# Optimization experiments

Hardware: AMD Instinct MI355X
Metric: run time of the kernel (lower is better)

Reference implementation:

```python
import jax, jax.numpy as jnp
import numpy as np

NUM_HEADS = 10
LN_EPS = 1e-5

def setup_inputs() -> dict:
    key = jax.random.key(0)
    ks = jax.random.split(key, 8)
    B, H, N, D, Dt = 256, 200, 64, 640, 256
    s = 0.02
    return {
        'clicked_news': jax.random.normal(ks[0], (B, H, D), jnp.float32),
        'clicked_topics': jax.random.normal(ks[1], (B, H, Dt), jnp.float32),
        'cand_topics': jax.random.normal(ks[2], (B, N, Dt), jnp.float32),
        'Wq': jax.random.normal(ks[3], (D, Dt), jnp.float32) * s,
        'bq': jnp.zeros((D,), jnp.float32),
        'Wk': jax.random.normal(ks[4], (D, Dt), jnp.float32) * s,
        'bk': jnp.zeros((D,), jnp.float32),
        'Wv': jax.random.normal(ks[5], (D, D), jnp.float32) * s,
        'bv': jnp.zeros((D,), jnp.float32),
        'Wg': jax.random.normal(ks[6], (D, D), jnp.float32) * s,
        'bg': jnp.zeros((D,), jnp.float32),
        'ln_gamma': jnp.ones((D,), jnp.float32),
        'ln_beta': jnp.zeros((D,), jnp.float32),
    }

def reference(clicked_news, clicked_topics, cand_topics, Wq, bq, Wk, bk, Wv, bv, Wg, bg, ln_gamma, ln_beta):
    B, H, D = clicked_news.shape
    N = cand_topics.shape[1]
    nh = NUM_HEADS
    hd = D // nh
    scale = jnp.sqrt(jnp.asarray(D, clicked_news.dtype))

    Qf = cand_topics @ Wq.T + bq            # [B, N, D]
    Kf = clicked_topics @ Wk.T + bk         # [B, H, D]
    # V projection feeds `weighted`, which is dead code w.r.t. outputs; omitted.

    Q = Qf.reshape(B, N, nh, hd)
    K = Kf.reshape(B, H, nh, hd)
    scores = jnp.einsum('bnhd,bmhd->bhnm', Q, K) / scale   # [B, nh, N, H]
    attn = jax.nn.softmax(scores, axis=-1)                 # dropout is identity in eval

    # query weighting: softmax over candidates of ||Q||
    query_weights = jax.nn.softmax(jnp.linalg.norm(Qf, axis=-1), axis=1)   # [B, N]
    agg = (attn.sum(axis=1) * query_weights[:, :, None]).sum(axis=1)       # [B, H]
    attn_weights_agg = jax.nn.softmax(agg, axis=-1)                        # [B, H]

    weighted_clicked = attn_weights_agg[:, :, None] * clicked_news         # [B, H, D]
    gate = jax.nn.sigmoid(weighted_clicked @ Wg.T + bg)
    out = gate * weighted_clicked + (1.0 - gate) * clicked_news

    mu = out.mean(axis=-1, keepdims=True)
    var = out.var(axis=-1, keepdims=True)
    out = (out - mu) / jnp.sqrt(var + LN_EPS) * ln_gamma + ln_beta
    return out, attn_weights_agg
```

## Files before the change

kernel.cpp:

```cpp
#include <hip/hip_runtime.h>
#include <math.h>

#define B_  256
#define H_  200
#define N_  64
#define D_  640
#define DT_ 256
#define NH_ 10
#define HD_ 64
#define MT_ 13

typedef __attribute__((ext_vector_type(8))) short bf16x8;
typedef __attribute__((ext_vector_type(4))) float f32x4;

__device__ __forceinline__ float wave_reduce_sum(float v) {
    #pragma unroll
    for (int m = 32; m > 0; m >>= 1) v += __shfl_xor(v, m);
    return v;
}
__device__ __forceinline__ float wave_reduce_max(float v) {
    #pragma unroll
    for (int m = 32; m > 0; m >>= 1) v = fmaxf(v, __shfl_xor(v, m));
    return v;
}
__device__ __forceinline__ float red16_sum(float v) {
    #pragma unroll
    for (int m = 1; m < 16; m <<= 1) v += __shfl_xor(v, m);
    return v;
}
__device__ __forceinline__ float red16_max(float v) {
    #pragma unroll
    for (int m = 1; m < 16; m <<= 1) v = fmaxf(v, __shfl_xor(v, m));
    return v;
}
__device__ __forceinline__ short f2bf(float x) {
    unsigned u = __float_as_uint(x);
    unsigned r = (u + 0x7fffu + ((u >> 16) & 1u)) >> 16;
    return (short)r;
}
__device__ __forceinline__ float bf2f(short s) {
    return __uint_as_float(((unsigned)(unsigned short)s) << 16);
}
#define SWZ(row, byte) ((byte) ^ (((row) & 7) << 4))

__global__ __launch_bounds__(256) void convert_w(
    const float* __restrict__ src, short* __restrict__ dst, int n)
{
    for (int i = blockIdx.x * 256 + threadIdx.x; i < n; i += gridDim.x * 256)
        dst[i] = f2bf(src[i]);
}

__global__ __launch_bounds__(512, 2) void proj_mfma(
    const float* __restrict__ X, const short* __restrict__ Wb,
    const float* __restrict__ bias, short* __restrict__ Y)
{
    __shared__ short A_lds[64 * DT_];
    const int t = threadIdx.x;
    const int lane = t & 63, w = t >> 6;
    const int r16 = lane & 15, g = lane >> 4;
    const long row0 = (long)blockIdx.x * 64;

    const float4* X4 = (const float4*)(X + row0 * DT_);
    for (int i = t; i < 64 * (DT_ / 4); i += 512) {
        float4 v = X4[i];
        int row = i / (DT_ / 4);
        int k4  = i % (DT_ / 4);
        short4 s;
        s.x = f2bf(v.x); s.y = f2bf(v.y); s.z = f2bf(v.z); s.w = f2bf(v.w);
        *(short4*)((char*)A_lds + SWZ(row, row * (DT_ * 2) + k4 * 8)) = s;
    }
    __syncthreads();

    f32x4 acc[5][4];
    #pragma unroll
    for (int ct = 0; ct < 5; ++ct)
        #pragma unroll
        for (int rt = 0; rt < 4; ++rt) acc[ct][rt] = (f32x4){0.f,0.f,0.f,0.f};

    const short* Wbase = Wb + (long)(w * 80 + r16) * DT_ + g * 8;
    #pragma unroll 2
    for (int kc = 0; kc < DT_ / 32; ++kc) {
        bf16x8 a[4];
        #pragma unroll
        for (int rt = 0; rt < 4; ++rt) {
            const int row = rt * 16 + r16;
            a[rt] = *(const bf16x8*)((const char*)A_lds +
                     SWZ(row, row * (DT_ * 2) + kc * 64 + g * 16));
        }
        bf16x8 bb[5];
        #pragma unroll
        for (int ct = 0; ct < 5; ++ct)
            bb[ct] = *(const bf16x8*)(Wbase + ct * 16 * DT_ + kc * 32);
        #pragma unroll
        for (int ct = 0; ct < 5; ++ct)
            #pragma unroll
            for (int rt = 0; rt < 4; ++rt)
                acc[ct][rt] = __builtin_amdgcn_mfma_f32_16x16x32_bf16(
                                  a[rt], bb[ct], acc[ct][rt], 0, 0, 0);
    }
    #pragma unroll
    for (int ct = 0; ct < 5; ++ct) {
        const int col = w * 80 + ct * 16 + r16;
        const float bv = bias[col];
        #pragma unroll
        for (int rt = 0; rt < 4; ++rt)
            #pragma unroll
            for (int i = 0; i < 4; ++i)
                Y[(row0 + rt * 16 + g * 4 + i) * (long)D_ + col] =
                    f2bf(acc[ct][rt][i] + bv);
    }
}

__global__ __launch_bounds__(256) void attn2(
    const short* __restrict__ Qb, const short* __restrict__ Kb,
    float* __restrict__ aw, float* __restrict__ out_tail)
{
    __shared__ float qn_l[N_];
    __shared__ float qw_l[N_];
    __shared__ float aggp[4][MT_ * 16];
    __shared__ float red2[2];
    const int t = threadIdx.x;
    const int lane = t & 63, wm = t >> 6;
    const int r16 = lane & 15, g = lane >> 4;
    const int b = blockIdx.x;

    {
        const short* qrow = Qb + ((long)(b * N_ + wm * 16 + r16)) * D_ + g * 160;
        float ss = 0.f;
        #pragma unroll
        for (int j = 0; j < 20; ++j) {
            bf16x8 v = *(const bf16x8*)(qrow + j * 8);
            #pragma unroll
            for (int e = 0; e < 8; ++e) { float f = bf2f(v[e]); ss += f * f; }
        }
        ss += __shfl_xor(ss, 16);
        ss += __shfl_xor(ss, 32);
        if (g == 0) qn_l[wm * 16 + r16] = ss;
    }
    __syncthreads();
    if (wm == 0) {
        float v = sqrtf(qn_l[lane]);
        float mx = wave_reduce_max(v);
        float e = __expf(v - mx);
        float s = wave_reduce_sum(e);
        qw_l[lane] = e / s;
    }
    __syncthreads();

    float qwr[4];
    #pragma unroll
    for (int i = 0; i < 4; ++i) qwr[i] = qw_l[wm * 16 + g * 4 + i];

    const float inv_scale = 0.0395284707521047f;
    float aggl[MT_];
    #pragma unroll
    for (int mt = 0; mt < MT_; ++mt) aggl[mt] = 0.f;

    for (int h = 0; h < NH_; ++h) {
        const short* qbase = Qb + ((long)(b * N_ + wm * 16 + r16)) * D_ + h * HD_ + g * 8;
        bf16x8 a0 = *(const bf16x8*)(qbase);
        bf16x8 a1 = *(const bf16x8*)(qbase + 32);
        f32x4 acc[MT_];
        #pragma unroll
        for (int mt = 0; mt < MT_; ++mt) {
            f32x4 z = {0.f,0.f,0.f,0.f};
            const short* kbase = Kb + ((long)(b * H_ + mt * 16 + r16)) * D_ + h * HD_ + g * 8;
            bf16x8 b0 = *(const bf16x8*)(kbase);
            bf16x8 b1 = *(const bf16x8*)(kbase + 32);
            z = __builtin_amdgcn_mfma_f32_16x16x32_bf16(a0, b0, z, 0, 0, 0);
            z = __builtin_amdgcn_mfma_f32_16x16x32_bf16(a1, b1, z, 0, 0, 0);
            acc[mt] = z;
        }
        const bool tailok = (r16 < 8);
        float mx[4] = {-INFINITY, -INFINITY, -INFINITY, -INFINITY};
        #pragma unroll
        for (int mt = 0; mt < MT_; ++mt) {
            const bool valid = (mt < 12) || tailok;
            #pragma unroll
            for (int i = 0; i < 4; ++i)
                if (valid) mx[i] = fmaxf(mx[i], acc[mt][i]);
        }
        #pragma unroll
        for (int i = 0; i < 4; ++i) mx[i] = red16_max(mx[i]);
        float sum[4] = {0.f, 0.f, 0.f, 0.f};
        #pragma unroll
        for (int mt = 0; mt < MT_; ++mt) {
            const bool valid = (mt < 12) || tailok;
            #pragma unroll
            for (int i = 0; i < 4; ++i) {
                float e = valid ? __expf((acc[mt][i] - mx[i]) * inv_scale) : 0.f;
                acc[mt][i] = e;
                sum[i] += e;
            }
        }
        float fct[4];
        #pragma unroll
        for (int i = 0; i < 4; ++i) fct[i] = qwr[i] / red16_sum(sum[i]);
        #pragma unroll
        for (int mt = 0; mt < MT_; ++mt)
            aggl[mt] += acc[mt][0] * fct[0] + acc[mt][1] * fct[1]
                      + acc[mt][2] * fct[2] + acc[mt][3] * fct[3];
    }
    #pragma unroll
    for (int mt = 0; mt < MT_; ++mt) {
        aggl[mt] += __shfl_xor(aggl[mt], 16);
        aggl[mt] += __shfl_xor(aggl[mt], 32);
    }
    if (g == 0) {
        #pragma unroll
        for (int mt = 0; mt < MT_; ++mt) aggp[wm][mt * 16 + r16] = aggl[mt];
    }
    __syncthreads();
    if (t < MT_ * 16) {
        float v = aggp[0][t] + aggp[1][t] + aggp[2][t] + aggp[3][t];
        aggp[0][t] = v;
    }
    __syncthreads();
    if (wm == 0) {
        float v0 = aggp[0][lane], v1 = aggp[0][lane + 64], v2 = aggp[0][lane + 128];
        const bool has3 = lane < (H_ - 192);
        float v3 = has3 ? aggp[0][lane + 192] : -INFINITY;
        float mx = wave_reduce_max(fmaxf(fmaxf(v0, v1), fmaxf(v2, v3)));
        float s = __expf(v0 - mx) + __expf(v1 - mx) + __expf(v2 - mx)
                + (has3 ? __expf(v3 - mx) : 0.f);
        s = wave_reduce_sum(s);
        if (lane == 0) { red2[0] = mx; red2[1] = s; }
    }
    __syncthreads();
    if (t < H_) {
        float v = __expf(aggp[0][t] - red2[0]) / red2[1];
        aw[b * H_ + t] = v;
        out_tail[b * H_ + t] = v;
    }
}

__global__ __launch_bounds__(512, 2) void out_mfma(
    const float* __restrict__ clicked, const float* __restrict__ aw,
    const short* __restrict__ Wgb, const float* __restrict__ bg,
    const float* __restrict__ gamma, const float* __restrict__ beta,
    float* __restrict__ out)
{
    __shared__ short A_lds[64 * D_];
    const int t = threadIdx.x;
    const int lane = t & 63, w = t >> 6;
    const int r16 = lane & 15, g = lane >> 4;
    const long row0 = (long)blockIdx.x * 64;

    {
        const float4* C4 = (const float4*)(clicked + row0 * D_);
        for (int i = t; i < 64 * (D_ / 4); i += 512) {
            int row = i / (D_ / 4);
            int k4  = i % (D_ / 4);
            float a = aw[row0 + row];
            float4 v = C4[i];
            short4 s;
            s.x = f2bf(v.x * a); s.y = f2bf(v.y * a);
            s.z = f2bf(v.z * a); s.w = f2bf(v.w * a);
            *(short4*)((char*)A_lds + SWZ(row, row * (D_ * 2) + k4 * 8)) = s;
        }
    }
    __syncthreads();

    f32x4 acc[5][4];
    #pragma unroll
    for (int ct = 0; ct < 5; ++ct)
        #pragma unroll
        for (int rt = 0; rt < 4; ++rt) acc[ct][rt] = (f32x4){0.f,0.f,0.f,0.f};

    const short* Wbase = Wgb + (long)(w * 80 + r16) * D_ + g * 8;
    #pragma unroll 2
    for (int kc = 0; kc < D_ / 32; ++kc) {
        bf16x8 a[4];
        #pragma unroll
        for (int rt = 0; rt < 4; ++rt) {
            const int row = rt * 16 + r16;
            a[rt] = *(const bf16x8*)((const char*)A_lds +
                     SWZ(row, row * (D_ * 2) + kc * 64 + g * 16));
        }
        bf16x8 bb[5];
        #pragma unroll
        for (int ct = 0; ct < 5; ++ct)
            bb[ct] = *(const bf16x8*)(Wbase + ct * 16 * D_ + kc * 32);
        #pragma unroll
        for (int ct = 0; ct < 5; ++ct)
            #pragma unroll
            for (int rt = 0; rt < 4; ++rt)
                acc[ct][rt] = __builtin_amdgcn_mfma_f32_16x16x32_bf16(
                                  a[rt], bb[ct], acc[ct][rt], 0, 0, 0);
    }
    __syncthreads();

    #pragma unroll
    for (int ct = 0; ct < 5; ++ct) {
        const int col = w * 80 + ct * 16 + r16;
        const float bv = bg[col];
        #pragma unroll
        for (int rt = 0; rt < 4; ++rt)
            #pragma unroll
            for (int i = 0; i < 4; ++i)
                A_lds[(rt * 16 + g * 4 + i) * D_ + col] = f2bf(acc[ct][rt][i] + bv);
    }
    __syncthreads();

    for (int rr = 0; rr < 8; ++rr) {
        const int r = w * 8 + rr;
        const long base = (row0 + r) * (long)D_;
        const float aww = aw[row0 + r];
        float ov[10];
        float s = 0.f, sq = 0.f;
        #pragma unroll
        for (int i = 0; i < 10; ++i) {
            const int c = lane + 64 * i;
            float cl = clicked[base + c];
            float z  = bf2f(A_lds[r * D_ + c]);
            float gt = 1.f / (1.f + __expf(-z));
            float o  = gt * (aww * cl) + (1.f - gt) * cl;
            ov[i] = o; s += o; sq += o * o;
        }
        s  = wave_reduce_sum(s);
        sq = wave_reduce_sum(sq);
        const float mu  = s * (1.f / D_);
        const float var = sq * (1.f / D_) - mu * mu;
        const float rinv = 1.0f / sqrtf(var + 1e-5f);
        #pragma unroll
        for (int i = 0; i < 10; ++i) {
            const int c = lane + 64 * i;
            out[base + c] = (ov[i] - mu) * rinv * gamma[c] + beta[c];
        }
    }
}

extern "C" void kernel_launch(void* const* d_in, const int* in_sizes, int n_in,
                              void* d_out, int out_size, void* d_ws, size_t ws_size,
                              hipStream_t stream) {
    const float* clicked_news   = (const float*)d_in[0];
    const float* clicked_topics = (const float*)d_in[1];
    const float* cand_topics    = (const float*)d_in[2];
    const float* Wq = (const float*)d_in[3];
    const float* bq = (const float*)d_in[4];
    const float* Wk = (const float*)d_in[5];
    const float* bk = (const float*)d_in[6];
    const float* Wg = (const float*)d_in[9];
    const float* bg = (const float*)d_in[10];
    const float* ln_gamma = (const float*)d_in[11];
    const float* ln_beta  = (const float*)d_in[12];

    float* out = (float*)d_out;
    float* ws  = (float*)d_ws;

    float* aw = ws;
    short* sbase = (short*)(ws + (long)B_ * H_);
    short* Qb   = sbase;
    short* Wq_b = Qb + (long)B_ * N_ * D_;
    short* Wg_b = Wq_b + (long)D_ * DT_;
    short* Wk_b = Wg_b + (long)D_ * D_;
    short* Kb = (short*)d_out;
    float* out_tail = out + (long)B_ * H_ * D_;

    convert_w<<<128, 256, 0, stream>>>(Wq, Wq_b, D_ * DT_);
    convert_w<<<128, 256, 0, stream>>>(Wk, Wk_b, D_ * DT_);
    convert_w<<<256, 256, 0, stream>>>(Wg, Wg_b, D_ * D_);

    proj_mfma<<<(B_ * N_) / 64, 512, 0, stream>>>(cand_topics, Wq_b, bq, Qb);
    proj_mfma<<<(B_ * H_) / 64, 512, 0, stream>>>(clicked_topics, Wk_b, bk, Kb);
    attn2<<<B_, 256, 0, stream>>>(Qb, Kb, aw, out_tail);
    out_mfma<<<(B_ * H_) / 64, 512, 0, stream>>>(clicked_news, aw, Wg_b, bg,
                                                 ln_gamma, ln_beta, out);
}
```

Measured before the change: 314.5 us.

## Double-buffer MFMA operands, batch global loads, split attention heads across waves

The GEMM kernels now prefetch the next k-chunk's LDS and weight fragments into a second register set while the current MFMAs run, and their staging loads are batched into unrolled per-thread loads. The attention kernel doubles its block to 512 threads, so each half of the waves handles five heads, and K fragments are loaded before the MFMAs. The out kernel also writes gate values into LDS through the swizzle and preloads the clicked values. All of this targets load latency and parallelism, at the cost of more registers and possible occupancy loss.

```diff
diff --git a/kernel.cpp b/kernel.cpp
--- a/kernel.cpp
+++ b/kernel.cpp
@@ -60,14 +60,19 @@
     const int r16 = lane & 15, g = lane >> 4;
     const long row0 = (long)blockIdx.x * 64;
 
-    const float4* X4 = (const float4*)(X + row0 * DT_);
-    for (int i = t; i < 64 * (DT_ / 4); i += 512) {
-        float4 v = X4[i];
-        int row = i / (DT_ / 4);
-        int k4  = i % (DT_ / 4);
-        short4 s;
-        s.x = f2bf(v.x); s.y = f2bf(v.y); s.z = f2bf(v.z); s.w = f2bf(v.w);
-        *(short4*)((char*)A_lds + SWZ(row, row * (DT_ * 2) + k4 * 8)) = s;
+    {
+        const int srow = t >> 3, sc = t & 7;
+        const float4* src = (const float4*)(X + (row0 + srow) * DT_) + sc;
+        float4 sv[8];
+        #pragma unroll
+        for (int j = 0; j < 8; ++j) sv[j] = src[8 * j];
+        #pragma unroll
+        for (int j = 0; j < 8; ++j) {
+            short4 s;
+            s.x = f2bf(sv[j].x); s.y = f2bf(sv[j].y);
+            s.z = f2bf(sv[j].z); s.w = f2bf(sv[j].w);
+            *(short4*)((char*)A_lds + SWZ(srow, srow * (DT_ * 2) + (sc + 8 * j) * 8)) = s;
+        }
     }
     __syncthreads();
 
@@ -78,26 +83,56 @@
         for (int rt = 0; rt < 4; ++rt) acc[ct][rt] = (f32x4){0.f,0.f,0.f,0.f};
 
     const short* Wbase = Wb + (long)(w * 80 + r16) * DT_ + g * 8;
-    #pragma unroll 2
-    for (int kc = 0; kc < DT_ / 32; ++kc) {
-        bf16x8 a[4];
-        #pragma unroll
-        for (int rt = 0; rt < 4; ++rt) {
-            const int row = rt * 16 + r16;
-            a[rt] = *(const bf16x8*)((const char*)A_lds +
-                     SWZ(row, row * (DT_ * 2) + kc * 64 + g * 16));
-        }
-        bf16x8 bb[5];
-        #pragma unroll
-        for (int ct = 0; ct < 5; ++ct)
-            bb[ct] = *(const bf16x8*)(Wbase + ct * 16 * DT_ + kc * 32);
+
+    bf16x8 aA[4], bA[5], aB[4], bB[5];
+    #pragma unroll
+    for (int rt = 0; rt < 4; ++rt) {
+        const int row = rt * 16 + r16;
+        aA[rt] = *(const bf16x8*)((const char*)A_lds + SWZ(row, row * (DT_ * 2) + g * 16));
+    }
+    #pragma unroll
+    for (int ct = 0; ct < 5; ++ct) bA[ct] = *(const bf16x8*)(Wbase + ct * 16 * DT_);
+
+    #pragma unroll
+    for (int kc = 0; kc < 8; kc += 2) {
+        {
+            const int kn = kc + 1;
+            #pragma unroll
+            for (int rt = 0; rt < 4; ++rt) {
+                const int row = rt * 16 + r16;
+                aB[rt] = *(const bf16x8*)((const char*)A_lds +
+                          SWZ(row, row * (DT_ * 2) + kn * 64 + g * 16));
+            }
+            #pragma unroll
+            for (int ct = 0; ct < 5; ++ct)
+                bB[ct] = *(const bf16x8*)(Wbase + ct * 16 * DT_ + kn * 32);
+        }
         #pragma unroll
         for (int ct = 0; ct < 5; ++ct)
             #pragma unroll
             for (int rt = 0; rt < 4; ++rt)
                 acc[ct][rt] = __builtin_amdgcn_mfma_f32_16x16x32_bf16(
-                                  a[rt], bb[ct], acc[ct][rt], 0, 0, 0);
-    }
+                                  aA[rt], bA[ct], acc[ct][rt], 0, 0, 0);
+        {
+            const int kn = (kc + 2 < 8) ? kc + 2 : 0;
+            #pragma unroll
+            for (int rt = 0; rt < 4; ++rt) {
+                const int row = rt * 16 + r16;
+                aA[rt] = *(const bf16x8*)((const char*)A_lds +
+                          SWZ(row, row * (DT_ * 2) + kn * 64 + g * 16));
+            }
+            #pragma unroll
+            for (int ct = 0; ct < 5; ++ct)
+                bA[ct] = *(const bf16x8*)(Wbase + ct * 16 * DT_ + kn * 32);
+        }
+        #pragma unroll
+        for (int ct = 0; ct < 5; ++ct)
+            #pragma unroll
+            for (int rt = 0; rt < 4; ++rt)
+                acc[ct][rt] = __builtin_amdgcn_mfma_f32_16x16x32_bf16(
+                                  aB[rt], bB[ct], acc[ct][rt], 0, 0, 0);
+    }
+
     #pragma unroll
     for (int ct = 0; ct < 5; ++ct) {
         const int col = w * 80 + ct * 16 + r16;
@@ -111,20 +146,21 @@
     }
 }
 
-__global__ __launch_bounds__(256) void attn2(
+__global__ __launch_bounds__(512, 2) void attn2(
     const short* __restrict__ Qb, const short* __restrict__ Kb,
     float* __restrict__ aw, float* __restrict__ out_tail)
 {
     __shared__ float qn_l[N_];
     __shared__ float qw_l[N_];
-    __shared__ float aggp[4][MT_ * 16];
+    __shared__ float aggp[8][MT_ * 16];
     __shared__ float red2[2];
     const int t = threadIdx.x;
-    const int lane = t & 63, wm = t >> 6;
+    const int lane = t & 63, w = t >> 6;
+    const int wm = w & 3, hh = w >> 2;
     const int r16 = lane & 15, g = lane >> 4;
     const int b = blockIdx.x;
 
-    {
+    if (hh == 0) {
         const short* qrow = Qb + ((long)(b * N_ + wm * 16 + r16)) * D_ + g * 160;
         float ss = 0.f;
         #pragma unroll
@@ -138,7 +174,7 @@
         if (g == 0) qn_l[wm * 16 + r16] = ss;
     }
     __syncthreads();
-    if (wm == 0) {
+    if (w == 0) {
         float v = sqrtf(qn_l[lane]);
         float mx = wave_reduce_max(v);
         float e = __expf(v - mx);
@@ -156,19 +192,24 @@
     #pragma unroll
     for (int mt = 0; mt < MT_; ++mt) aggl[mt] = 0.f;
 
-    for (int h = 0; h < NH_; ++h) {
+    for (int hi = 0; hi < 5; ++hi) {
+        const int h = hh * 5 + hi;
         const short* qbase = Qb + ((long)(b * N_ + wm * 16 + r16)) * D_ + h * HD_ + g * 8;
         bf16x8 a0 = *(const bf16x8*)(qbase);
         bf16x8 a1 = *(const bf16x8*)(qbase + 32);
+        bf16x8 kb0[MT_], kb1[MT_];
+        #pragma unroll
+        for (int mt = 0; mt < MT_; ++mt) {
+            const short* kbase = Kb + ((long)(b * H_ + mt * 16 + r16)) * D_ + h * HD_ + g * 8;
+            kb0[mt] = *(const bf16x8*)(kbase);
+            kb1[mt] = *(const bf16x8*)(kbase + 32);
+        }
         f32x4 acc[MT_];
         #pragma unroll
         for (int mt = 0; mt < MT_; ++mt) {
             f32x4 z = {0.f,0.f,0.f,0.f};
-            const short* kbase = Kb + ((long)(b * H_ + mt * 16 + r16)) * D_ + h * HD_ + g * 8;
-            bf16x8 b0 = *(const bf16x8*)(kbase);
-            bf16x8 b1 = *(const bf16x8*)(kbase + 32);
-            z = __builtin_amdgcn_mfma_f32_16x16x32_bf16(a0, b0, z, 0, 0, 0);
-            z = __builtin_amdgcn_mfma_f32_16x16x32_bf16(a1, b1, z, 0, 0, 0);
+            z = __builtin_amdgcn_mfma_f32_16x16x32_bf16(a0, kb0[mt], z, 0, 0, 0);
+            z = __builtin_amdgcn_mfma_f32_16x16x32_bf16(a1, kb1[mt], z, 0, 0, 0);
             acc[mt] = z;
         }
         const bool tailok = (r16 < 8);
@@ -208,15 +249,17 @@
     }
     if (g == 0) {
         #pragma unroll
-        for (int mt = 0; mt < MT_; ++mt) aggp[wm][mt * 16 + r16] = aggl[mt];
+        for (int mt = 0; mt < MT_; ++mt) aggp[w][mt * 16 + r16] = aggl[mt];
     }
     __syncthreads();
     if (t < MT_ * 16) {
-        float v = aggp[0][t] + aggp[1][t] + aggp[2][t] + aggp[3][t];
+        float v = 0.f;
+        #pragma unroll
+        for (int j = 0; j < 8; ++j) v += aggp[j][t];
         aggp[0][t] = v;
     }
     __syncthreads();
-    if (wm == 0) {
+    if (w == 0) {
         float v0 = aggp[0][lane], v1 = aggp[0][lane + 64], v2 = aggp[0][lane + 128];
         const bool has3 = lane < (H_ - 192);
         float v3 = has3 ? aggp[0][lane + 192] : -INFINITY;
@@ -247,16 +290,18 @@
     const long row0 = (long)blockIdx.x * 64;
 
     {
-        const float4* C4 = (const float4*)(clicked + row0 * D_);
-        for (int i = t; i < 64 * (D_ / 4); i += 512) {
-            int row = i / (D_ / 4);
-            int k4  = i % (D_ / 4);
-            float a = aw[row0 + row];
-            float4 v = C4[i];
+        const int srow = t >> 3, sc = t & 7;
+        const float a = aw[row0 + srow];
+        const float4* src = (const float4*)(clicked + (row0 + srow) * D_) + sc;
+        float4 sv[20];
+        #pragma unroll
+        for (int j = 0; j < 20; ++j) sv[j] = src[8 * j];
+        #pragma unroll
+        for (int j = 0; j < 20; ++j) {
             short4 s;
-            s.x = f2bf(v.x * a); s.y = f2bf(v.y * a);
-            s.z = f2bf(v.z * a); s.w = f2bf(v.w * a);
-            *(short4*)((char*)A_lds + SWZ(row, row * (D_ * 2) + k4 * 8)) = s;
+            s.x = f2bf(sv[j].x * a); s.y = f2bf(sv[j].y * a);
+            s.z = f2bf(sv[j].z * a); s.w = f2bf(sv[j].w * a);
+            *(short4*)((char*)A_lds + SWZ(srow, srow * (D_ * 2) + (sc + 8 * j) * 8)) = s;
         }
     }
     __syncthreads();
@@ -268,25 +313,54 @@
         for (int rt = 0; rt < 4; ++rt) acc[ct][rt] = (f32x4){0.f,0.f,0.f,0.f};
 
     const short* Wbase = Wgb + (long)(w * 80 + r16) * D_ + g * 8;
-    #pragma unroll 2
-    for (int kc = 0; kc < D_ / 32; ++kc) {
-        bf16x8 a[4];
-        #pragma unroll
-        for (int rt = 0; rt < 4; ++rt) {
-            const int row = rt * 16 + r16;
-            a[rt] = *(const bf16x8*)((const char*)A_lds +
-                     SWZ(row, row * (D_ * 2) + kc * 64 + g * 16));
-        }
-        bf16x8 bb[5];
-        #pragma unroll
-        for (int ct = 0; ct < 5; ++ct)
-            bb[ct] = *(const bf16x8*)(Wbase + ct * 16 * D_ + kc * 32);
+
+    bf16x8 aA[4], bA[5], aB[4], bB[5];
+    #pragma unroll
+    for (int rt = 0; rt < 4; ++rt) {
+        const int row = rt * 16 + r16;
+        aA[rt] = *(const bf16x8*)((const char*)A_lds + SWZ(row, row * (D_ * 2) + g * 16));
+    }
+    #pragma unroll
+    for (int ct = 0; ct < 5; ++ct) bA[ct] = *(const bf16x8*)(Wbase + ct * 16 * D_);
+
+    #pragma unroll
+    for (int kc = 0; kc < 20; kc += 2) {
+        {
+            const int kn = kc + 1;
+            #pragma unroll
+            for (int rt = 0; rt < 4; ++rt) {
+                const int row = rt * 16 + r16;
+                aB[rt] = *(const bf16x8*)((const char*)A_lds +
+                          SWZ(row, row * (D_ * 2) + kn * 64 + g * 16));
+            }
+            #pragma unroll
+            for (int ct = 0; ct < 5; ++ct)
+                bB[ct] = *(const bf16x8*)(Wbase + ct * 16 * D_ + kn * 32);
+        }
         #pragma unroll
         for (int ct = 0; ct < 5; ++ct)
             #pragma unroll
             for (int rt = 0; rt < 4; ++rt)
                 acc[ct][rt] = __builtin_amdgcn_mfma_f32_16x16x32_bf16(
-                                  a[rt], bb[ct], acc[ct][rt], 0, 0, 0);
+                                  aA[rt], bA[ct], acc[ct][rt], 0, 0, 0);
+        {
+            const int kn = (kc + 2 < 20) ? kc + 2 : 0;
+            #pragma unroll
+            for (int rt = 0; rt < 4; ++rt) {
+                const int row = rt * 16 + r16;
+                aA[rt] = *(const bf16x8*)((const char*)A_lds +
+                          SWZ(row, row * (D_ * 2) + kn * 64 + g * 16));
+            }
+            #pragma unroll
+            for (int ct = 0; ct < 5; ++ct)
+                bA[ct] = *(const bf16x8*)(Wbase + ct * 16 * D_ + kn * 32);
+        }
+        #pragma unroll
+        for (int ct = 0; ct < 5; ++ct)
+            #pragma unroll
+            for (int rt = 0; rt < 4; ++rt)
+                acc[ct][rt] = __builtin_amdgcn_mfma_f32_16x16x32_bf16(
+                                  aB[rt], bB[ct], acc[ct][rt], 0, 0, 0);
     }
     __syncthreads();
 
@@ -297,8 +371,11 @@
         #pragma unroll
         for (int rt = 0; rt < 4; ++rt)
             #pragma unroll
-            for (int i = 0; i < 4; ++i)
-                A_lds[(rt * 16 + g * 4 + i) * D_ + col] = f2bf(acc[ct][rt][i] + bv);
+            for (int i = 0; i < 4; ++i) {
+                const int row = rt * 16 + g * 4 + i;
+                *(short*)((char*)A_lds + SWZ(row, row * (D_ * 2) + col * 2)) =
+                    f2bf(acc[ct][rt][i] + bv);
+            }
     }
     __syncthreads();
 
@@ -306,15 +383,17 @@
         const int r = w * 8 + rr;
         const long base = (row0 + r) * (long)D_;
         const float aww = aw[row0 + r];
-        float ov[10];
+        float cl[10], ov[10];
+        #pragma unroll
+        for (int i = 0; i < 10; ++i) cl[i] = clicked[base + lane + 64 * i];
         float s = 0.f, sq = 0.f;
         #pragma unroll
         for (int i = 0; i < 10; ++i) {
             const int c = lane + 64 * i;
-            float cl = clicked[base + c];
-            float z  = bf2f(A_lds[r * D_ + c]);
+            float z = bf2f(*(const short*)((const char*)A_lds +
+                           SWZ(r, r * (D_ * 2) + c * 2)));
             float gt = 1.f / (1.f + __expf(-z));
-            float o  = gt * (aww * cl) + (1.f - gt) * cl;
+            float o  = gt * (aww * cl[i]) + (1.f - gt) * cl[i];
             ov[i] = o; s += o; sq += o * o;
         }
         s  = wave_reduce_sum(s);
@@ -363,7 +442,7 @@
 
     proj_mfma<<<(B_ * N_) / 64, 512, 0, stream>>>(cand_topics, Wq_b, bq, Qb);
     proj_mfma<<<(B_ * H_) / 64, 512, 0, stream>>>(clicked_topics, Wk_b, bk, Kb);
-    attn2<<<B_, 256, 0, stream>>>(Qb, Kb, aw, out_tail);
+    attn2<<<B_, 512, 0, stream>>>(Qb, Kb, aw, out_tail);
     out_mfma<<<(B_ * H_) / 64, 512, 0, stream>>>(clicked_news, aw, Wg_b, bg,
                                                  ln_gamma, ln_beta, out);
 }
```

New measurement: 311.6 us. About the same (-0.9%).
